# Performance work log

Hardware: AMD Instinct MI355X
Metric: run time of the kernel (lower is better)

## Reference

```python
import jax, jax.numpy as jnp
import numpy as np

EPS = 1e-5
NEG_SLOPE = 0.2  # DGL GATConv default leaky_relu slope


def conv1d_same(x, w, b):
    # x: [N, Cin, T], w: [Cout, Cin, K]
    y = jax.lax.conv_general_dilated(x, w, (1,), 'SAME',
                                     dimension_numbers=('NCW', 'OIW', 'NCW'))
    return y + b[None, :, None]


def gated_conv(x, w1, b1, w2, b2, w3, b3):
    # Temporal_Gated_Conv: relu(conv1(x)*sigmoid(conv2(x)) + conv3(x))
    return jax.nn.relu(conv1d_same(x, w1, b1) * jax.nn.sigmoid(conv1d_same(x, w2, b2))
                       + conv1d_same(x, w3, b3))


def bn3(x, g, b):
    # BatchNorm1d on [N, C, T]: stats over (N, T), training mode (batch stats)
    m = jnp.mean(x, (0, 2), keepdims=True)
    v = jnp.var(x, (0, 2), keepdims=True)
    return (x - m) * jax.lax.rsqrt(v + EPS) * g[None, :, None] + b[None, :, None]


def bn2(x, g, b):
    # BatchNorm1d on [N, F]: stats over N
    m = jnp.mean(x, 0, keepdims=True)
    v = jnp.var(x, 0, keepdims=True)
    return (x - m) * jax.lax.rsqrt(v + EPS) * g[None, :] + b[None, :]


def setup_inputs() -> dict:
    key = jax.random.key(0)
    ks = jax.random.split(key, 24)
    N, C, T, H, DEG = 20000, 32, 8, 4, 16
    F = C * T          # GAT in/out feats per head = 256
    E = N * DEG
    s = 0.05
    inp = {
        'X': jax.random.normal(ks[0], (N, C, T), jnp.float32),
        'src': jax.random.randint(ks[1], (E,), 0, N, jnp.int32),
        'dst': jax.random.randint(ks[2], (E,), 0, N, jnp.int32),
        # residual_proj: Conv1d(C->C, k=1)
        'rp_w': jax.random.normal(ks[3], (C, C, 1), jnp.float32) * s,
        'rp_b': jnp.zeros((C,), jnp.float32),
        # gated_conv1: three Conv1d(C->C, k=3)
        'g1_w1': jax.random.normal(ks[4], (C, C, 3), jnp.float32) * s,
        'g1_b1': jnp.zeros((C,), jnp.float32),
        'g1_w2': jax.random.normal(ks[5], (C, C, 3), jnp.float32) * s,
        'g1_b2': jnp.zeros((C,), jnp.float32),
        'g1_w3': jax.random.normal(ks[6], (C, C, 3), jnp.float32) * s,
        'g1_b3': jnp.zeros((C,), jnp.float32),
        'bn0_g': jnp.ones((C,), jnp.float32),
        'bn0_b': jnp.zeros((C,), jnp.float32),
        # GATConv: fc [H*F, F], attn_l/attn_r [H, F], bias [H*F]
        'gat_w': jax.random.normal(ks[7], (H * F, F), jnp.float32) * s,
        'attn_l': jax.random.normal(ks[8], (H, F), jnp.float32) * s,
        'attn_r': jax.random.normal(ks[9], (H, F), jnp.float32) * s,
        'gat_bias': jnp.zeros((H * F,), jnp.float32),
        'bn1_g': jnp.ones((H * F,), jnp.float32),
        'bn1_b': jnp.zeros((H * F,), jnp.float32),
        # gated_conv2: three Conv1d(C*H -> C, k=3)
        'g2_w1': jax.random.normal(ks[10], (C, C * H, 3), jnp.float32) * s,
        'g2_b1': jnp.zeros((C,), jnp.float32),
        'g2_w2': jax.random.normal(ks[11], (C, C * H, 3), jnp.float32) * s,
        'g2_b2': jnp.zeros((C,), jnp.float32),
        'g2_w3': jax.random.normal(ks[12], (C, C * H, 3), jnp.float32) * s,
        'g2_b3': jnp.zeros((C,), jnp.float32),
        'bn2_g': jnp.ones((C,), jnp.float32),
        'bn2_b': jnp.zeros((C,), jnp.float32),
    }
    return inp


def reference(X, src, dst, rp_w, rp_b, g1_w1, g1_b1, g1_w2, g1_b2, g1_w3, g1_b3,
              bn0_g, bn0_b, gat_w, attn_l, attn_r, gat_bias, bn1_g, bn1_b,
              g2_w1, g2_b1, g2_w2, g2_b2, g2_w3, g2_b3, bn2_g, bn2_b):
    N, C, T = X.shape
    H, F = attn_l.shape

    residual = conv1d_same(X, rp_w, rp_b)                      # [N, C, T]
    x = gated_conv(X, g1_w1, g1_b1, g1_w2, g1_b2, g1_w3, g1_b3)
    x = bn3(x, bn0_g, bn0_b)
    x = x.reshape(N, C * T)                                    # row-major flatten == torch .view

    # --- DGL GATConv (feat_drop=attn_drop=0, concat heads, ReLU activation) ---
    h = (x @ gat_w.T).reshape(N, H, F)                         # fc projection
    el = jnp.sum(h * attn_l, -1)                               # [N, H]
    er = jnp.sum(h * attn_r, -1)                               # [N, H]
    e = jax.nn.leaky_relu(el[src] + er[dst], NEG_SLOPE)        # [E, H]
    # segment softmax over incoming edges of each dst node
    m = jax.ops.segment_max(e, dst, num_segments=N)            # [N, H]
    ee = jnp.exp(e - m[dst])
    den = jax.ops.segment_sum(ee, dst, num_segments=N)         # [N, H]
    alpha = ee / den[dst]                                      # [E, H]
    rst = jax.ops.segment_sum(alpha[:, :, None] * h[src], dst, num_segments=N)  # [N, H, F]
    rst = jax.nn.relu(rst + gat_bias.reshape(H, F))

    x = rst.reshape(N, H * F)                                  # concat heads
    x = bn2(x, bn1_g, bn1_b)
    x = x.reshape(N, (H * F) // T, T)                          # [N, C*H, T]
    x = gated_conv(x, g2_w1, g2_b1, g2_w2, g2_b2, g2_w3, g2_b3)
    x = bn3(x, bn2_g, bn2_b)
    x = jax.nn.relu(x + residual)                              # self.last=True, dropout=0
    return x
```

## Files before the change

### kernel.cpp

```cpp
#include <hip/hip_runtime.h>
#include <stdint.h>

#define NN 20000
#define NE 320000

typedef unsigned short us16;
typedef __attribute__((ext_vector_type(8))) short short8;
typedef __attribute__((ext_vector_type(4))) float f32x4;

union U4 { uint4 v; us16 s[8]; unsigned u[4]; };
union U2 { uint2 v; us16 s[4]; };

__device__ __forceinline__ float b2f(us16 u){ return __uint_as_float(((unsigned)u)<<16); }
__device__ __forceinline__ us16 f2b(float f){
  unsigned u = __float_as_uint(f);
  u += 0x7fffu + ((u>>16)&1u);
  return (us16)(u>>16);
}

__global__ __launch_bounds__(256) void k_misc(
    const float* __restrict__ gatw, us16* __restrict__ Wb,
    const float* __restrict__ w1, const float* __restrict__ w2, const float* __restrict__ w3,
    us16* __restrict__ Wt,
    const float* __restrict__ c1w1, const float* __restrict__ c1w2, const float* __restrict__ c1w3,
    const float* __restrict__ rp_w, us16* __restrict__ Wt1,
    const float* __restrict__ attnl, const float* __restrict__ attnr,
    float* __restrict__ wl, float* __restrict__ wr,
    const int* __restrict__ dst, int* __restrict__ counts)
{
  const int b = blockIdx.x, tid = threadIdx.x;
  if(b < 256){
    int i = b*256 + tid;
    float4 v = *(const float4*)(gatw + (size_t)i*4);
    U2 o;
    o.s[0]=f2b(v.x); o.s[1]=f2b(v.y); o.s[2]=f2b(v.z); o.s[3]=f2b(v.w);
    *(uint2*)(Wb + (size_t)i*4) = o.v;
  } else if(b < 400){
    int i = (b-256)*256 + tid;
    int s = i/12288, rem = i%12288;
    int co3 = rem>>7, ci = rem&127;
    const float* w = (co3<32) ? w1 : (co3<64) ? w2 : w3;
    Wt[i] = f2b(w[(co3&31)*384 + ci*3 + s]);
  } else if(b < 448){
    int i = (b-400)*256 + tid;
    int s = i>>12, rem = i&4095;
    int co3 = rem>>5, ci = rem&31;
    float v;
    if(co3 < 96){
      const float* w = (co3<32) ? c1w1 : (co3<64) ? c1w2 : c1w3;
      v = w[(co3&31)*96 + ci*3 + s];
    } else {
      v = (s==1) ? rp_w[(co3-96)*32 + ci] : 0.f;
    }
    Wt1[i] = f2b(v);
  } else if(b < 456){
    int bb = b-448;
    int sel = bb>>2, hd = bb&3, k = tid;
    const float* attn = sel ? attnr : attnl;
    float s = 0.f;
    for(int f=0; f<256; f++)
      s = fmaf(attn[hd*256+f], gatw[(size_t)(hd*256+f)*256 + k], s);
    (sel ? wr : wl)[hd*256+k] = s;
  } else {
    int e = (b-456)*256 + tid;
    if(e < NE) atomicAdd(&counts[dst[e]], 1);
  }
}

__global__ __launch_bounds__(256) void k_gemm1(
    const float* __restrict__ X, const us16* __restrict__ Wt1,
    const float* __restrict__ b1, const float* __restrict__ b2, const float* __restrict__ b3,
    const float* __restrict__ rp_b,
    us16* __restrict__ gc1, us16* __restrict__ resid,
    float* __restrict__ bn0_sum, float* __restrict__ bn0_sq)
{
  __shared__ float smemF[16896];
  us16* As = (us16*)smemF;
  us16* Bs = As + 6400;
  float* Cs = smemF;
  __shared__ float redS[32], redQ[32];
  const int tid = threadIdx.x;
  if(tid<32){ redS[tid]=0.f; redQ[tid]=0.f; }
  const int node0 = blockIdx.x*16;
  const int lane = tid&63, wv = tid>>6;
  const int wm = wv&1, wn = wv>>1;
  const int mrow = lane&15, kg = (lane>>4)*8;
  for(int idx=tid; idx<1024; idx+=256){
    int n = idx>>6, rem = idx&63, slot = (rem>>5)*9, ci = rem&31;
    As[n*400 + slot*40 + ci] = 0;
  }
  #pragma unroll
  for(int i=0;i<4;i++){
    int idx = i*256 + tid;
    int n = idx>>6, rem = idx&63, ci = rem>>1, tq = rem&1;
    float4 xv = *(const float4*)(X + (size_t)(node0+n)*256 + ci*8 + tq*4);
    us16* p = &As[n*400 + (tq*4+1)*40 + ci];
    p[0]   = f2b(xv.x);
    p[40]  = f2b(xv.y);
    p[80]  = f2b(xv.z);
    p[120] = f2b(xv.w);
  }
  #pragma unroll
  for(int i=0;i<6;i++){
    int c = i*256 + tid;
    int s = c>>9, rem = c&511, co = rem>>2, cq = rem&3;
    *(uint4*)&Bs[s*5120 + co*40 + cq*8] = *(const uint4*)(Wt1 + s*4096 + co*32 + cq*8);
  }
  __syncthreads();
  f32x4 acc[4][4] = {};
  #pragma unroll
  for(int s=0; s<3; s++){
    short8 af[4], bfr[4];
    #pragma unroll
    for(int i=0;i<4;i++){
      int r = wm*64 + i*16 + mrow;
      af[i] = *(const short8*)&As[(r>>3)*400 + ((r&7)+s)*40 + kg];
    }
    #pragma unroll
    for(int j=0;j<4;j++)
      bfr[j] = *(const short8*)&Bs[s*5120 + (wn*64 + j*16 + mrow)*40 + kg];
    #pragma unroll
    for(int i=0;i<4;i++){
      #pragma unroll
      for(int j=0;j<4;j++)
        acc[i][j] = __builtin_amdgcn_mfma_f32_16x16x32_bf16(af[i], bfr[j], acc[i][j], 0, 0, 0);
    }
  }
  __syncthreads();
  #pragma unroll
  for(int i=0;i<4;i++){
    #pragma unroll
    for(int j=0;j<4;j++){
      #pragma unroll
      for(int r=0;r<4;r++)
        Cs[(wm*64 + i*16 + (lane>>4)*4 + r)*132 + wn*64 + j*16 + (lane&15)] = acc[i][j][r];
    }
  }
  __syncthreads();
  const int co = tid&31, rg = tid>>5;
  const float bb1=b1[co], bb2=b2[co], bb3=b3[co], bbr=rp_b[co];
  float s=0.f, q=0.f;
  #pragma unroll
  for(int half=0; half<2; half++){
    U4 ov, rv;
    #pragma unroll
    for(int t=0;t<8;t++){
      int r = rg*16 + half*8 + t;
      float c1 = Cs[r*132 + co]      + bb1;
      float c2 = Cs[r*132 + co + 32] + bb2;
      float c3 = Cs[r*132 + co + 64] + bb3;
      float rr = Cs[r*132 + co + 96] + bbr;
      float sg = 1.f/(1.f+__expf(-c2));
      float v = fmaf(c1, sg, c3);
      v = v>0.f ? v : 0.f;
      s += v; q += v*v;
      ov.s[t] = f2b(v);
      rv.s[t] = f2b(rr);
    }
    int node = node0 + rg*2 + half;
    *(uint4*)(gc1   + (size_t)node*256 + co*8) = ov.v;
    *(uint4*)(resid + (size_t)node*256 + co*8) = rv.v;
  }
  atomicAdd(&redS[co], s); atomicAdd(&redQ[co], q);
  __syncthreads();
  if(tid<32)      atomicAdd(&bn0_sum[tid], redS[tid]);
  else if(tid<64) atomicAdd(&bn0_sq[tid-32], redQ[tid-32]);
}

__global__ __launch_bounds__(256) void k_eler2(const us16* __restrict__ gc1,
    const float* __restrict__ bn0_sum, const float* __restrict__ bn0_sq,
    const float* __restrict__ bn0g, const float* __restrict__ bn0b,
    const float* __restrict__ wl, const float* __restrict__ wr,
    float* __restrict__ el, float* __restrict__ er)
{
  __shared__ float sa[32], sb[32];
  const int tid = threadIdx.x;
  if(tid<32){
    float m = bn0_sum[tid]*(1.f/160000.f);
    float v = bn0_sq[tid]*(1.f/160000.f) - m*m;
    float a = bn0g[tid]*rsqrtf(v + 1e-5f);
    sa[tid] = a; sb[tid] = bn0b[tid] - m*a;
  }
  __syncthreads();
  const int wv = tid>>6, lane = tid&63;
  const int node = blockIdx.x*4 + wv;
  U2 g; g.v = *(const uint2*)(gc1 + (size_t)node*256 + lane*4);
  const float a = sa[lane>>1], b = sb[lane>>1];
  float xv[4];
  #pragma unroll
  for(int j=0;j<4;j++) xv[j] = fmaf(a, b2f(g.s[j]), b);
  float res[8];
  #pragma unroll
  for(int hd=0; hd<4; hd++){
    float4 lv = *(const float4*)(wl + hd*256 + lane*4);
    float4 rv = *(const float4*)(wr + hd*256 + lane*4);
    res[hd]   = xv[0]*lv.x + xv[1]*lv.y + xv[2]*lv.z + xv[3]*lv.w;
    res[4+hd] = xv[0]*rv.x + xv[1]*rv.y + xv[2]*rv.z + xv[3]*rv.w;
  }
  #pragma unroll
  for(int o=32;o;o>>=1){
    #pragma unroll
    for(int k=0;k<8;k++) res[k] += __shfl_xor(res[k], o, 64);
  }
  if(lane==0){
    #pragma unroll
    for(int hd=0;hd<4;hd++){ el[node*4+hd]=res[hd]; er[node*4+hd]=res[4+hd]; }
  }
}

__global__ __launch_bounds__(1024) void k_scan(const int* __restrict__ counts,
                                               int* __restrict__ offsets, int* __restrict__ cursor)
{
  __shared__ int buf[1024];
  const int tid = threadIdx.x;
  const int base = tid*20;
  int loc[20];
  int s = 0;
  #pragma unroll
  for(int j=0;j<20;j++){
    int idx = base+j;
    int v = (idx<NN) ? counts[idx] : 0;
    loc[j] = s; s += v;
  }
  buf[tid] = s;
  __syncthreads();
  for(int off=1; off<1024; off<<=1){
    int t = (tid>=off) ? buf[tid-off] : 0;
    __syncthreads();
    buf[tid] += t;
    __syncthreads();
  }
  int excl = buf[tid] - s;
  #pragma unroll
  for(int j=0;j<20;j++){
    int idx = base+j;
    if(idx<NN){ offsets[idx]=excl+loc[j]; cursor[idx]=excl+loc[j]; }
  }
  if(tid==1023) offsets[NN] = excl + s;
}

__global__ __launch_bounds__(256) void k_scatter(const int* __restrict__ src, const int* __restrict__ dst,
    int* __restrict__ cursor, int* __restrict__ esrc,
    const float* __restrict__ el, const float* __restrict__ er,
    float* __restrict__ ew)
{
  int e = blockIdx.x*256 + threadIdx.x;
  if(e < NE){
    int s = src[e], d = dst[e];
    int pos = atomicAdd(&cursor[d], 1);
    esrc[pos] = s;
    float4 lv = *(const float4*)(el + s*4);
    float4 rv = *(const float4*)(er + d*4);
    float4 sc;
    sc.x = lv.x+rv.x; sc.x = sc.x>0.f ? sc.x : 0.2f*sc.x;
    sc.y = lv.y+rv.y; sc.y = sc.y>0.f ? sc.y : 0.2f*sc.y;
    sc.z = lv.z+rv.z; sc.z = sc.z>0.f ? sc.z : 0.2f*sc.z;
    sc.w = lv.w+rv.w; sc.w = sc.w>0.f ? sc.w : 0.2f*sc.w;
    *(float4*)(ew + (size_t)pos*4) = sc;
  }
}

__global__ __launch_bounds__(256) void k_agg2(
    const int* __restrict__ offsets, const int* __restrict__ esrc,
    const float* __restrict__ ew, const us16* __restrict__ gc1,
    const float* __restrict__ bn0_sum, const float* __restrict__ bn0_sq,
    const float* __restrict__ bn0g, const float* __restrict__ bn0b,
    us16* __restrict__ Axg)
{
  const int tid = threadIdx.x;
  const int wv = tid>>6, lane = tid&63;
  const int node = blockIdx.x*4 + wv;
  const int ch = lane>>1;
  float mmn = bn0_sum[ch]*(1.f/160000.f);
  float vvn = bn0_sq[ch]*(1.f/160000.f) - mmn*mmn;
  float sa = bn0g[ch]*rsqrtf(vvn + 1e-5f);
  float sb = bn0b[ch] - mmn*sa;
  const int beg = offsets[node];
  const int deg = offsets[node+1] - beg;
  const int h = lane>>4, i0 = lane&15;
  float m = -3.0e38f;
  for(int i=i0; i<deg; i+=16) m = fmaxf(m, ew[(size_t)(beg+i)*4 + h]);
  m = fmaxf(m, __shfl_xor(m,1,64)); m = fmaxf(m, __shfl_xor(m,2,64));
  m = fmaxf(m, __shfl_xor(m,4,64)); m = fmaxf(m, __shfl_xor(m,8,64));
  float den = 0.f;
  for(int i=i0; i<deg; i+=16) den += __expf(ew[(size_t)(beg+i)*4 + h] - m);
  den += __shfl_xor(den,1,64); den += __shfl_xor(den,2,64);
  den += __shfl_xor(den,4,64); den += __shfl_xor(den,8,64);
  const float m0=__shfl(m,0,64),   m1=__shfl(m,16,64),  m2=__shfl(m,32,64),  m3=__shfl(m,48,64);
  const float d0=__shfl(den,0,64), d1=__shfl(den,16,64),d2=__shfl(den,32,64),d3=__shfl(den,48,64);
  const float v0=d0>0.f?1.f/d0:0.f, v1=d1>0.f?1.f/d1:0.f,
              v2=d2>0.f?1.f/d2:0.f, v3=d3>0.f?1.f/d3:0.f;
  float a0c[4]={},a1c[4]={},a2c[4]={},a3c[4]={};
  #pragma unroll 4
  for(int j=0; j<deg; j++){
    int pos = beg+j;
    float4 w4 = *(const float4*)(ew + (size_t)pos*4);
    int sN = esrc[pos];
    U2 hv; hv.v = *(const uint2*)(gc1 + (size_t)sN*256 + lane*4);
    float e0 = __expf(w4.x-m0)*v0;
    float e1 = __expf(w4.y-m1)*v1;
    float e2 = __expf(w4.z-m2)*v2;
    float e3 = __expf(w4.w-m3)*v3;
    #pragma unroll
    for(int kk=0;kk<4;kk++){
      float x = b2f(hv.s[kk]);
      a0c[kk] = fmaf(e0,x,a0c[kk]);
      a1c[kk] = fmaf(e1,x,a1c[kk]);
      a2c[kk] = fmaf(e2,x,a2c[kk]);
      a3c[kk] = fmaf(e3,x,a3c[kk]);
    }
  }
  const float sbi = sb * ((deg>0)?1.f:0.f);
  U2 o0,o1,o2,o3;
  #pragma unroll
  for(int kk=0;kk<4;kk++){
    o0.s[kk]=f2b(fmaf(sa,a0c[kk],sbi));
    o1.s[kk]=f2b(fmaf(sa,a1c[kk],sbi));
    o2.s[kk]=f2b(fmaf(sa,a2c[kk],sbi));
    o3.s[kk]=f2b(fmaf(sa,a3c[kk],sbi));
  }
  *(uint2*)(Axg + ((size_t)node)*256            + lane*4) = o0.v;
  *(uint2*)(Axg + ((size_t)NN + node)*256       + lane*4) = o1.v;
  *(uint2*)(Axg + ((size_t)2*NN + node)*256     + lane*4) = o2.v;
  *(uint2*)(Axg + ((size_t)3*NN + node)*256     + lane*4) = o3.v;
}

__global__ __launch_bounds__(256) void k_gemm3(const us16* __restrict__ Axg, const us16* __restrict__ Wb,
    const float* __restrict__ gbias, us16* __restrict__ rst,
    float* __restrict__ bn1_sum, float* __restrict__ bn1_sq)
{
  __shared__ us16 As[128*72];
  __shared__ us16 Bs[128*72];
  const int tid = threadIdx.x;
  const int row0 = blockIdx.x*128;
  const int cb   = blockIdx.y*128;
  const int hd   = blockIdx.z;
  const us16* A = Axg + (size_t)hd*NN*256;
  const us16* B = Wb  + (size_t)(hd*256 + cb)*256;
  const int lane = tid&63, wv = tid>>6;
  const int wm = wv&1, wn = wv>>1;
  const int mrow = lane&15, kg = (lane>>4)*8;
  f32x4 acc[4][4] = {};
  for(int k0=0; k0<256; k0+=64){
    #pragma unroll
    for(int i=0;i<4;i++){
      int chunk = i*256 + tid;
      int row = chunk>>3, cc = chunk&7;
      int g = row0 + row;
      uint4 av; av.x=0;av.y=0;av.z=0;av.w=0;
      if(g < NN) av = *(const uint4*)(A + (size_t)g*256 + k0 + cc*8);
      *(uint4*)&As[row*72 + cc*8] = av;
      *(uint4*)&Bs[row*72 + cc*8] = *(const uint4*)(B + (size_t)row*256 + k0 + cc*8);
    }
    __syncthreads();
    #pragma unroll
    for(int kk=0; kk<64; kk+=32){
      short8 af[4], bfr[4];
      #pragma unroll
      for(int i=0;i<4;i++) af[i]  = *(const short8*)&As[(wm*64 + i*16 + mrow)*72 + kk + kg];
      #pragma unroll
      for(int j=0;j<4;j++) bfr[j] = *(const short8*)&Bs[(wn*64 + j*16 + mrow)*72 + kk + kg];
      #pragma unroll
      for(int i=0;i<4;i++){
        #pragma unroll
        for(int j=0;j<4;j++)
          acc[i][j] = __builtin_amdgcn_mfma_f32_16x16x32_bf16(af[i], bfr[j], acc[i][j], 0, 0, 0);
      }
    }
    __syncthreads();
  }
  float gb[4];
  #pragma unroll
  for(int j=0;j<4;j++)
    gb[j] = gbias[hd*256 + cb + wn*64 + j*16 + (lane&15)];
  float cs[4]={}, cq[4]={};
  #pragma unroll
  for(int i=0;i<4;i++){
    #pragma unroll
    for(int j=0;j<4;j++){
      #pragma unroll
      for(int r=0;r<4;r++){
        int g = row0 + wm*64 + i*16 + (lane>>4)*4 + r;
        if(g < NN){
          float v = acc[i][j][r] + gb[j];
          v = v>0.f ? v : 0.f;
          rst[(size_t)g*1024 + hd*256 + cb + wn*64 + j*16 + (lane&15)] = f2b(v);
          cs[j] += v; cq[j] += v*v;
        }
      }
    }
  }
  #pragma unroll
  for(int j=0;j<4;j++){
    cs[j] += __shfl_xor(cs[j],16,64); cs[j] += __shfl_xor(cs[j],32,64);
    cq[j] += __shfl_xor(cq[j],16,64); cq[j] += __shfl_xor(cq[j],32,64);
  }
  if(lane < 16){
    #pragma unroll
    for(int j=0;j<4;j++){
      int col = hd*256 + cb + wn*64 + j*16 + lane;
      atomicAdd(&bn1_sum[col], cs[j]);
      atomicAdd(&bn1_sq[col],  cq[j]);
    }
  }
}

__global__ __launch_bounds__(256) void k_gemm2(
    const us16* __restrict__ rst, const us16* __restrict__ Wt,
    const float* __restrict__ bn1_sum, const float* __restrict__ bn1_sq,
    const float* __restrict__ bn1g, const float* __restrict__ bn1b,
    const float* __restrict__ b1, const float* __restrict__ b2, const float* __restrict__ b3,
    us16* __restrict__ y2, float* __restrict__ bn2_sum, float* __restrict__ bn2_sq)
{
  __shared__ float smemF[16384];
  float* s1a = smemF;
  float* s1b = smemF + 1024;
  us16* As = (us16*)(smemF + 2048);
  us16* Bs = As + 21760;
  float* Cs = (float*)(smemF + 2048);
  __shared__ float redS[32], redQ[32];
  const int tid = threadIdx.x;
  if(tid<32){ redS[tid]=0.f; redQ[tid]=0.f; }
  const int node0 = blockIdx.x*16;
  const int lane = tid&63, wv = tid>>6;
  const int wm = wv&1, wn = wv>>1;
  const int mrow = lane&15, kg = (lane>>4)*8;
  for(int f=tid; f<1024; f+=256){
    float m = bn1_sum[f]*(1.f/20000.f);
    float v = bn1_sq[f]*(1.f/20000.f) - m*m;
    float a = bn1g[f]*rsqrtf(v + 1e-5f);
    int l = (f&7)*128 + (f>>3);
    s1a[l] = a; s1b[l] = bn1b[f] - m*a;
  }
  for(int idx=tid; idx<4096; idx+=256){
    int n = idx>>8, rem = idx&255, slot = (rem>>7)*9, ci = rem&127;
    As[n*1360 + slot*136 + ci] = 0;
  }
  __syncthreads();
  #pragma unroll
  for(int i=0;i<8;i++){
    int idx = i*256 + tid;
    int n = idx>>7, ci = idx&127;
    U4 in; in.v = *(const uint4*)(rst + (size_t)(node0+n)*1024 + ci*8);
    us16* p = &As[n*1360 + 136 + ci];
    #pragma unroll
    for(int t=0;t<8;t++){
      float a = s1a[t*128+ci], b = s1b[t*128+ci];
      p[t*136] = f2b(fmaf(a, b2f(in.s[t]), b));
    }
  }
  f32x4 acc[4][3] = {};
  for(int rd=0; rd<6; rd++){
    const int s = rd>>1, kc = rd&1;
    __syncthreads();
    #pragma unroll
    for(int i=0;i<3;i++){
      int chunk = i*256 + tid;
      int brow = chunk>>3, cc = chunk&7;
      *(uint4*)&Bs[brow*72 + cc*8] =
        *(const uint4*)(Wt + s*12288 + brow*128 + kc*64 + cc*8);
    }
    __syncthreads();
    #pragma unroll
    for(int kk=0; kk<64; kk+=32){
      short8 af[4], bfr[3];
      #pragma unroll
      for(int i=0;i<4;i++){
        int r = wm*64 + i*16 + mrow;
        af[i] = *(const short8*)&As[(r>>3)*1360 + ((r&7)+s)*136 + kc*64 + kk + kg];
      }
      #pragma unroll
      for(int j=0;j<3;j++)
        bfr[j] = *(const short8*)&Bs[(wn*48 + j*16 + mrow)*72 + kk + kg];
      #pragma unroll
      for(int i=0;i<4;i++){
        #pragma unroll
        for(int j=0;j<3;j++)
          acc[i][j] = __builtin_amdgcn_mfma_f32_16x16x32_bf16(af[i], bfr[j], acc[i][j], 0, 0, 0);
      }
    }
  }
  __syncthreads();
  #pragma unroll
  for(int i=0;i<4;i++){
    #pragma unroll
    for(int j=0;j<3;j++){
      #pragma unroll
      for(int r=0;r<4;r++)
        Cs[(wm*64 + i*16 + (lane>>4)*4 + r)*100 + wn*48 + j*16 + (lane&15)] = acc[i][j][r];
    }
  }
  __syncthreads();
  const int co = tid&31, rg = tid>>5;
  const float bb1=b1[co], bb2=b2[co], bb3=b3[co];
  float s=0.f, q=0.f;
  #pragma unroll
  for(int half=0; half<2; half++){
    U4 ov;
    #pragma unroll
    for(int t=0;t<8;t++){
      int r = rg*16 + half*8 + t;
      float c1 = Cs[r*100 + co]      + bb1;
      float c2 = Cs[r*100 + co + 32] + bb2;
      float c3 = Cs[r*100 + co + 64] + bb3;
      float sg = 1.f/(1.f+__expf(-c2));
      float v = fmaf(c1, sg, c3);
      v = v>0.f ? v : 0.f;
      s += v; q += v*v;
      ov.s[t] = f2b(v);
    }
    int node = node0 + rg*2 + half;
    *(uint4*)(y2 + (size_t)node*256 + co*8) = ov.v;
  }
  atomicAdd(&redS[co], s); atomicAdd(&redQ[co], q);
  __syncthreads();
  if(tid<32)      atomicAdd(&bn2_sum[tid], redS[tid]);
  else if(tid<64) atomicAdd(&bn2_sq[tid-32], redQ[tid-32]);
}

__global__ __launch_bounds__(256) void k_final(const us16* __restrict__ y2,
    const float* __restrict__ bn2_sum, const float* __restrict__ bn2_sq,
    const float* __restrict__ bn2g, const float* __restrict__ bn2b,
    const us16* __restrict__ resid, float* __restrict__ out)
{
  __shared__ float fa[32], fb[32];
  const int tid = threadIdx.x;
  if(tid<32){
    float m = bn2_sum[tid]*(1.f/160000.f);
    float v = bn2_sq[tid]*(1.f/160000.f) - m*m;
    float a = bn2g[tid]*rsqrtf(v + 1e-5f);
    fa[tid] = a; fb[tid] = bn2b[tid] - m*a;
  }
  __syncthreads();
  size_t base = ((size_t)blockIdx.x*256 + tid)*8;
  int ch = (int)((base>>3)&31);
  float a = fa[ch], b = fb[ch];
  U4 yv, rv;
  yv.v = *(const uint4*)(y2+base);
  rv.v = *(const uint4*)(resid+base);
  float4 o0, o1;
  float vv[8];
  #pragma unroll
  for(int j=0;j<8;j++){
    float v = fmaf(a, b2f(yv.s[j]), b) + b2f(rv.s[j]);
    vv[j] = v>0.f ? v : 0.f;
  }
  o0.x=vv[0]; o0.y=vv[1]; o0.z=vv[2]; o0.w=vv[3];
  o1.x=vv[4]; o1.y=vv[5]; o1.z=vv[6]; o1.w=vv[7];
  *(float4*)(out+base)   = o0;
  *(float4*)(out+base+4) = o1;
}

extern "C" void kernel_launch(void* const* d_in, const int* in_sizes, int n_in,
                              void* d_out, int out_size, void* d_ws, size_t ws_size,
                              hipStream_t stream)
{
  const float* X    = (const float*)d_in[0];
  const int*  src   = (const int*)d_in[1];
  const int*  dst   = (const int*)d_in[2];
  const float* rp_w = (const float*)d_in[3];
  const float* rp_b = (const float*)d_in[4];
  const float* g1w1 = (const float*)d_in[5];
  const float* g1b1 = (const float*)d_in[6];
  const float* g1w2 = (const float*)d_in[7];
  const float* g1b2 = (const float*)d_in[8];
  const float* g1w3 = (const float*)d_in[9];
  const float* g1b3 = (const float*)d_in[10];
  const float* bn0g = (const float*)d_in[11];
  const float* bn0b = (const float*)d_in[12];
  const float* gatw = (const float*)d_in[13];
  const float* attnl= (const float*)d_in[14];
  const float* attnr= (const float*)d_in[15];
  const float* gbias= (const float*)d_in[16];
  const float* bn1g = (const float*)d_in[17];
  const float* bn1b = (const float*)d_in[18];
  const float* g2w1 = (const float*)d_in[19];
  const float* g2b1 = (const float*)d_in[20];
  const float* g2w2 = (const float*)d_in[21];
  const float* g2b2 = (const float*)d_in[22];
  const float* g2w3 = (const float*)d_in[23];
  const float* g2b3 = (const float*)d_in[24];
  const float* bn2g = (const float*)d_in[25];
  const float* bn2b = (const float*)d_in[26];
  float* out = (float*)d_out;
  (void)in_sizes; (void)n_in; (void)out_size; (void)ws_size;

  char* w = (char*)d_ws;
  float* bn0_sum = (float*)w;
  float* bn0_sq  = bn0_sum + 32;
  float* bn1_sum = bn0_sum + 64;
  float* bn1_sq  = bn1_sum + 1024;
  float* bn2_sum = bn1_sq  + 1024;
  float* bn2_sq  = bn2_sum + 32;
  int*   counts  = (int*)(bn2_sq + 32);
  size_t zeroBytes = (size_t)((char*)(counts + NN) - w);
  int*   offsets = counts + NN;
  int*   cursor  = offsets + 20004;
  int*   esrc    = cursor + NN;
  float* el      = (float*)(esrc + NE);
  float* er      = el + NN*4;
  float* ew      = er + NN*4;
  float* wl      = ew + (size_t)NE*4;
  float* wr      = wl + 1024;
  us16*  wb      = (us16*)(wr + 1024);
  us16*  resid   = wb + 262144;
  us16*  gc1     = resid + 5120000;
  us16*  Axg     = gc1   + 5120000;
  us16*  rst     = Axg   + 20480000;
  us16*  Wt      = rst   + 20480000;
  us16*  Wt1     = Wt    + 36864;
  us16*  y2      = gc1;

  hipMemsetAsync(d_ws, 0, zeroBytes, stream);
  k_misc<<<1706, 256, 0, stream>>>(gatw, wb, g2w1, g2w2, g2w3, Wt,
                                   g1w1, g1w2, g1w3, rp_w, Wt1,
                                   attnl, attnr, wl, wr, dst, counts);
  k_gemm1<<<1250, 256, 0, stream>>>(X, Wt1, g1b1, g1b2, g1b3, rp_b,
                                    gc1, resid, bn0_sum, bn0_sq);
  k_eler2<<<5000, 256, 0, stream>>>(gc1, bn0_sum, bn0_sq, bn0g, bn0b, wl, wr, el, er);
  k_scan<<<1, 1024, 0, stream>>>(counts, offsets, cursor);
  k_scatter<<<1250, 256, 0, stream>>>(src, dst, cursor, esrc, el, er, ew);
  k_agg2<<<5000, 256, 0, stream>>>(offsets, esrc, ew, gc1, bn0_sum, bn0_sq, bn0g, bn0b, Axg);
  k_gemm3<<<dim3(157, 2, 4), 256, 0, stream>>>(Axg, wb, gbias, rst, bn1_sum, bn1_sq);
  k_gemm2<<<1250, 256, 0, stream>>>(rst, Wt, bn1_sum, bn1_sq, bn1g, bn1b,
                                    g2b1, g2b2, g2b3, y2, bn2_sum, bn2_sq);
  k_final<<<2500, 256, 0, stream>>>(y2, bn2_sum, bn2_sq, bn2g, bn2b, resid, out);
}
```

Baseline: 393.0 us.

## Fuse scan into el/er kernel, widen GAT GEMM tile to full head

The single-block prefix scan now runs as an extra block appended to the el/er kernel, which removes one launch and its serialization. The scan uses 256 threads with 79 nodes each. The GAT projection GEMM now computes a 128x256 tile per block, covering all 256 columns of a head, so each A tile is loaded once instead of twice. This doubles the accumulator registers and the B shared-memory footprint, which may reduce occupancy. An unroll pragma is also added to the attention-weight precompute loop.

```diff
diff --git a/kernel.cpp b/kernel.cpp
--- a/kernel.cpp
+++ b/kernel.cpp
@@ -58,6 +58,7 @@
     int sel = bb>>2, hd = bb&3, k = tid;
     const float* attn = sel ? attnr : attnl;
     float s = 0.f;
+    #pragma unroll 8
     for(int f=0; f<256; f++)
       s = fmaf(attn[hd*256+f], gatw[(size_t)(hd*256+f)*256 + k], s);
     (sel ? wr : wl)[hd*256+k] = s;
@@ -171,72 +172,69 @@
     const float* __restrict__ bn0_sum, const float* __restrict__ bn0_sq,
     const float* __restrict__ bn0g, const float* __restrict__ bn0b,
     const float* __restrict__ wl, const float* __restrict__ wr,
-    float* __restrict__ el, float* __restrict__ er)
-{
-  __shared__ float sa[32], sb[32];
+    float* __restrict__ el, float* __restrict__ er,
+    const int* __restrict__ counts, int* __restrict__ offsets, int* __restrict__ cursor)
+{
   const int tid = threadIdx.x;
-  if(tid<32){
-    float m = bn0_sum[tid]*(1.f/160000.f);
-    float v = bn0_sq[tid]*(1.f/160000.f) - m*m;
-    float a = bn0g[tid]*rsqrtf(v + 1e-5f);
-    sa[tid] = a; sb[tid] = bn0b[tid] - m*a;
-  }
-  __syncthreads();
-  const int wv = tid>>6, lane = tid&63;
-  const int node = blockIdx.x*4 + wv;
-  U2 g; g.v = *(const uint2*)(gc1 + (size_t)node*256 + lane*4);
-  const float a = sa[lane>>1], b = sb[lane>>1];
-  float xv[4];
-  #pragma unroll
-  for(int j=0;j<4;j++) xv[j] = fmaf(a, b2f(g.s[j]), b);
-  float res[8];
-  #pragma unroll
-  for(int hd=0; hd<4; hd++){
-    float4 lv = *(const float4*)(wl + hd*256 + lane*4);
-    float4 rv = *(const float4*)(wr + hd*256 + lane*4);
-    res[hd]   = xv[0]*lv.x + xv[1]*lv.y + xv[2]*lv.z + xv[3]*lv.w;
-    res[4+hd] = xv[0]*rv.x + xv[1]*rv.y + xv[2]*rv.z + xv[3]*rv.w;
-  }
-  #pragma unroll
-  for(int o=32;o;o>>=1){
-    #pragma unroll
-    for(int k=0;k<8;k++) res[k] += __shfl_xor(res[k], o, 64);
-  }
-  if(lane==0){
-    #pragma unroll
-    for(int hd=0;hd<4;hd++){ el[node*4+hd]=res[hd]; er[node*4+hd]=res[4+hd]; }
-  }
-}
-
-__global__ __launch_bounds__(1024) void k_scan(const int* __restrict__ counts,
-                                               int* __restrict__ offsets, int* __restrict__ cursor)
-{
-  __shared__ int buf[1024];
-  const int tid = threadIdx.x;
-  const int base = tid*20;
-  int loc[20];
-  int s = 0;
-  #pragma unroll
-  for(int j=0;j<20;j++){
-    int idx = base+j;
-    int v = (idx<NN) ? counts[idx] : 0;
-    loc[j] = s; s += v;
-  }
-  buf[tid] = s;
-  __syncthreads();
-  for(int off=1; off<1024; off<<=1){
-    int t = (tid>=off) ? buf[tid-off] : 0;
+  if(blockIdx.x < 5000){
+    __shared__ float sa[32], sb[32];
+    if(tid<32){
+      float m = bn0_sum[tid]*(1.f/160000.f);
+      float v = bn0_sq[tid]*(1.f/160000.f) - m*m;
+      float a = bn0g[tid]*rsqrtf(v + 1e-5f);
+      sa[tid] = a; sb[tid] = bn0b[tid] - m*a;
+    }
     __syncthreads();
-    buf[tid] += t;
+    const int wv = tid>>6, lane = tid&63;
+    const int node = blockIdx.x*4 + wv;
+    U2 g; g.v = *(const uint2*)(gc1 + (size_t)node*256 + lane*4);
+    const float a = sa[lane>>1], b = sb[lane>>1];
+    float xv[4];
+    #pragma unroll
+    for(int j=0;j<4;j++) xv[j] = fmaf(a, b2f(g.s[j]), b);
+    float res[8];
+    #pragma unroll
+    for(int hd=0; hd<4; hd++){
+      float4 lv = *(const float4*)(wl + hd*256 + lane*4);
+      float4 rv = *(const float4*)(wr + hd*256 + lane*4);
+      res[hd]   = xv[0]*lv.x + xv[1]*lv.y + xv[2]*lv.z + xv[3]*lv.w;
+      res[4+hd] = xv[0]*rv.x + xv[1]*rv.y + xv[2]*rv.z + xv[3]*rv.w;
+    }
+    #pragma unroll
+    for(int o=32;o;o>>=1){
+      #pragma unroll
+      for(int k=0;k<8;k++) res[k] += __shfl_xor(res[k], o, 64);
+    }
+    if(lane==0){
+      #pragma unroll
+      for(int hd=0;hd<4;hd++){ el[node*4+hd]=res[hd]; er[node*4+hd]=res[4+hd]; }
+    }
+  } else {
+    __shared__ int buf[256];
+    const int base = tid*79;
+    int s = 0;
+    for(int j=0;j<79;j++){
+      int idx = base+j;
+      if(idx<NN) s += counts[idx];
+    }
+    buf[tid] = s;
     __syncthreads();
-  }
-  int excl = buf[tid] - s;
-  #pragma unroll
-  for(int j=0;j<20;j++){
-    int idx = base+j;
-    if(idx<NN){ offsets[idx]=excl+loc[j]; cursor[idx]=excl+loc[j]; }
-  }
-  if(tid==1023) offsets[NN] = excl + s;
+    for(int off=1; off<256; off<<=1){
+      int t = (tid>=off) ? buf[tid-off] : 0;
+      __syncthreads();
+      buf[tid] += t;
+      __syncthreads();
+    }
+    int excl = buf[tid] - s;
+    for(int j=0;j<79;j++){
+      int idx = base+j;
+      if(idx<NN){
+        offsets[idx]=excl; cursor[idx]=excl;
+        excl += counts[idx];
+      }
+    }
+    if(tid==255) offsets[NN] = buf[255];
+  }
 }
 
 __global__ __launch_bounds__(256) void k_scatter(const int* __restrict__ src, const int* __restrict__ dst,
@@ -330,17 +328,16 @@
     float* __restrict__ bn1_sum, float* __restrict__ bn1_sq)
 {
   __shared__ us16 As[128*72];
-  __shared__ us16 Bs[128*72];
+  __shared__ us16 Bs[256*72];
   const int tid = threadIdx.x;
   const int row0 = blockIdx.x*128;
-  const int cb   = blockIdx.y*128;
-  const int hd   = blockIdx.z;
+  const int hd   = blockIdx.y;
   const us16* A = Axg + (size_t)hd*NN*256;
-  const us16* B = Wb  + (size_t)(hd*256 + cb)*256;
+  const us16* B = Wb  + (size_t)hd*256*256;
   const int lane = tid&63, wv = tid>>6;
   const int wm = wv&1, wn = wv>>1;
   const int mrow = lane&15, kg = (lane>>4)*8;
-  f32x4 acc[4][4] = {};
+  f32x4 acc[4][8] = {};
   for(int k0=0; k0<256; k0+=64){
     #pragma unroll
     for(int i=0;i<4;i++){
@@ -350,55 +347,60 @@
       uint4 av; av.x=0;av.y=0;av.z=0;av.w=0;
       if(g < NN) av = *(const uint4*)(A + (size_t)g*256 + k0 + cc*8);
       *(uint4*)&As[row*72 + cc*8] = av;
+    }
+    #pragma unroll
+    for(int i=0;i<8;i++){
+      int chunk = i*256 + tid;
+      int row = chunk>>3, cc = chunk&7;
       *(uint4*)&Bs[row*72 + cc*8] = *(const uint4*)(B + (size_t)row*256 + k0 + cc*8);
     }
     __syncthreads();
     #pragma unroll
     for(int kk=0; kk<64; kk+=32){
-      short8 af[4], bfr[4];
+      short8 af[4], bfr[8];
       #pragma unroll
       for(int i=0;i<4;i++) af[i]  = *(const short8*)&As[(wm*64 + i*16 + mrow)*72 + kk + kg];
       #pragma unroll
-      for(int j=0;j<4;j++) bfr[j] = *(const short8*)&Bs[(wn*64 + j*16 + mrow)*72 + kk + kg];
+      for(int j=0;j<8;j++) bfr[j] = *(const short8*)&Bs[(wn*128 + j*16 + mrow)*72 + kk + kg];
       #pragma unroll
       for(int i=0;i<4;i++){
         #pragma unroll
-        for(int j=0;j<4;j++)
+        for(int j=0;j<8;j++)
           acc[i][j] = __builtin_amdgcn_mfma_f32_16x16x32_bf16(af[i], bfr[j], acc[i][j], 0, 0, 0);
       }
     }
     __syncthreads();
   }
-  float gb[4];
-  #pragma unroll
-  for(int j=0;j<4;j++)
-    gb[j] = gbias[hd*256 + cb + wn*64 + j*16 + (lane&15)];
-  float cs[4]={}, cq[4]={};
+  float gb[8];
+  #pragma unroll
+  for(int j=0;j<8;j++)
+    gb[j] = gbias[hd*256 + wn*128 + j*16 + (lane&15)];
+  float cs[8]={}, cq[8]={};
   #pragma unroll
   for(int i=0;i<4;i++){
     #pragma unroll
-    for(int j=0;j<4;j++){
+    for(int j=0;j<8;j++){
       #pragma unroll
       for(int r=0;r<4;r++){
         int g = row0 + wm*64 + i*16 + (lane>>4)*4 + r;
         if(g < NN){
           float v = acc[i][j][r] + gb[j];
           v = v>0.f ? v : 0.f;
-          rst[(size_t)g*1024 + hd*256 + cb + wn*64 + j*16 + (lane&15)] = f2b(v);
+          rst[(size_t)g*1024 + hd*256 + wn*128 + j*16 + (lane&15)] = f2b(v);
           cs[j] += v; cq[j] += v*v;
         }
       }
     }
   }
   #pragma unroll
-  for(int j=0;j<4;j++){
+  for(int j=0;j<8;j++){
     cs[j] += __shfl_xor(cs[j],16,64); cs[j] += __shfl_xor(cs[j],32,64);
     cq[j] += __shfl_xor(cq[j],16,64); cq[j] += __shfl_xor(cq[j],32,64);
   }
   if(lane < 16){
     #pragma unroll
-    for(int j=0;j<4;j++){
-      int col = hd*256 + cb + wn*64 + j*16 + lane;
+    for(int j=0;j<8;j++){
+      int col = hd*256 + wn*128 + j*16 + lane;
       atomicAdd(&bn1_sum[col], cs[j]);
       atomicAdd(&bn1_sq[col],  cq[j]);
     }
@@ -617,11 +619,11 @@
                                    attnl, attnr, wl, wr, dst, counts);
   k_gemm1<<<1250, 256, 0, stream>>>(X, Wt1, g1b1, g1b2, g1b3, rp_b,
                                     gc1, resid, bn0_sum, bn0_sq);
-  k_eler2<<<5000, 256, 0, stream>>>(gc1, bn0_sum, bn0_sq, bn0g, bn0b, wl, wr, el, er);
-  k_scan<<<1, 1024, 0, stream>>>(counts, offsets, cursor);
+  k_eler2<<<5001, 256, 0, stream>>>(gc1, bn0_sum, bn0_sq, bn0g, bn0b, wl, wr, el, er,
+                                    counts, offsets, cursor);
   k_scatter<<<1250, 256, 0, stream>>>(src, dst, cursor, esrc, el, er, ew);
   k_agg2<<<5000, 256, 0, stream>>>(offsets, esrc, ew, gc1, bn0_sum, bn0_sq, bn0g, bn0b, Axg);
-  k_gemm3<<<dim3(157, 2, 4), 256, 0, stream>>>(Axg, wb, gbias, rst, bn1_sum, bn1_sq);
+  k_gemm3<<<dim3(157, 4), 256, 0, stream>>>(Axg, wb, gbias, rst, bn1_sum, bn1_sq);
   k_gemm2<<<1250, 256, 0, stream>>>(rst, Wt, bn1_sum, bn1_sq, bn1g, bn1b,
                                     g2b1, g2b2, g2b3, y2, bn2_sum, bn2_sq);
   k_final<<<2500, 256, 0, stream>>>(y2, bn2_sum, bn2_sq, bn2g, bn2b, resid, out);
```

Measured after the change: 445.3 us. 1.13x slower.

## Fuse scan into eler kernel, split attn-weight reduction, shrink gemm3 K tile

Applied to the files above, without the earlier changes.

The single-block scan is folded into the el/er kernel as an extra block, which removes one kernel launch. It now uses 256 threads instead of 1024 and does a serial 79-element pass that rereads counts. The attention-weight folding in k_misc is split four ways over f, with atomicAdd into wl/wr, which are moved into the zeroed workspace region. gemm3 now uses a 32-wide K tile with smaller shared-memory buffers, which may raise occupancy but doubles the number of barriers.

```diff
diff --git a/kernel.cpp b/kernel.cpp
--- a/kernel.cpp
+++ b/kernel.cpp
@@ -53,16 +53,19 @@
       v = (s==1) ? rp_w[(co3-96)*32 + ci] : 0.f;
     }
     Wt1[i] = f2b(v);
-  } else if(b < 456){
+  } else if(b < 480){
     int bb = b-448;
-    int sel = bb>>2, hd = bb&3, k = tid;
+    int sel = bb>>4, hd = (bb>>2)&3, fq = bb&3;
     const float* attn = sel ? attnr : attnl;
+    int k = tid;
     float s = 0.f;
-    for(int f=0; f<256; f++)
+    int f0 = fq*64;
+    #pragma unroll 8
+    for(int f=f0; f<f0+64; f++)
       s = fmaf(attn[hd*256+f], gatw[(size_t)(hd*256+f)*256 + k], s);
-    (sel ? wr : wl)[hd*256+k] = s;
+    atomicAdd(&((sel ? wr : wl)[hd*256+k]), s);
   } else {
-    int e = (b-456)*256 + tid;
+    int e = (b-480)*256 + tid;
     if(e < NE) atomicAdd(&counts[dst[e]], 1);
   }
 }
@@ -171,72 +174,69 @@
     const float* __restrict__ bn0_sum, const float* __restrict__ bn0_sq,
     const float* __restrict__ bn0g, const float* __restrict__ bn0b,
     const float* __restrict__ wl, const float* __restrict__ wr,
-    float* __restrict__ el, float* __restrict__ er)
-{
-  __shared__ float sa[32], sb[32];
+    float* __restrict__ el, float* __restrict__ er,
+    const int* __restrict__ counts, int* __restrict__ offsets, int* __restrict__ cursor)
+{
   const int tid = threadIdx.x;
-  if(tid<32){
-    float m = bn0_sum[tid]*(1.f/160000.f);
-    float v = bn0_sq[tid]*(1.f/160000.f) - m*m;
-    float a = bn0g[tid]*rsqrtf(v + 1e-5f);
-    sa[tid] = a; sb[tid] = bn0b[tid] - m*a;
-  }
-  __syncthreads();
-  const int wv = tid>>6, lane = tid&63;
-  const int node = blockIdx.x*4 + wv;
-  U2 g; g.v = *(const uint2*)(gc1 + (size_t)node*256 + lane*4);
-  const float a = sa[lane>>1], b = sb[lane>>1];
-  float xv[4];
-  #pragma unroll
-  for(int j=0;j<4;j++) xv[j] = fmaf(a, b2f(g.s[j]), b);
-  float res[8];
-  #pragma unroll
-  for(int hd=0; hd<4; hd++){
-    float4 lv = *(const float4*)(wl + hd*256 + lane*4);
-    float4 rv = *(const float4*)(wr + hd*256 + lane*4);
-    res[hd]   = xv[0]*lv.x + xv[1]*lv.y + xv[2]*lv.z + xv[3]*lv.w;
-    res[4+hd] = xv[0]*rv.x + xv[1]*rv.y + xv[2]*rv.z + xv[3]*rv.w;
-  }
-  #pragma unroll
-  for(int o=32;o;o>>=1){
-    #pragma unroll
-    for(int k=0;k<8;k++) res[k] += __shfl_xor(res[k], o, 64);
-  }
-  if(lane==0){
-    #pragma unroll
-    for(int hd=0;hd<4;hd++){ el[node*4+hd]=res[hd]; er[node*4+hd]=res[4+hd]; }
-  }
-}
-
-__global__ __launch_bounds__(1024) void k_scan(const int* __restrict__ counts,
-                                               int* __restrict__ offsets, int* __restrict__ cursor)
-{
-  __shared__ int buf[1024];
-  const int tid = threadIdx.x;
-  const int base = tid*20;
-  int loc[20];
-  int s = 0;
-  #pragma unroll
-  for(int j=0;j<20;j++){
-    int idx = base+j;
-    int v = (idx<NN) ? counts[idx] : 0;
-    loc[j] = s; s += v;
-  }
-  buf[tid] = s;
-  __syncthreads();
-  for(int off=1; off<1024; off<<=1){
-    int t = (tid>=off) ? buf[tid-off] : 0;
+  if(blockIdx.x < 5000){
+    __shared__ float sa[32], sb[32];
+    if(tid<32){
+      float m = bn0_sum[tid]*(1.f/160000.f);
+      float v = bn0_sq[tid]*(1.f/160000.f) - m*m;
+      float a = bn0g[tid]*rsqrtf(v + 1e-5f);
+      sa[tid] = a; sb[tid] = bn0b[tid] - m*a;
+    }
     __syncthreads();
-    buf[tid] += t;
+    const int wv = tid>>6, lane = tid&63;
+    const int node = blockIdx.x*4 + wv;
+    U2 g; g.v = *(const uint2*)(gc1 + (size_t)node*256 + lane*4);
+    const float a = sa[lane>>1], b = sb[lane>>1];
+    float xv[4];
+    #pragma unroll
+    for(int j=0;j<4;j++) xv[j] = fmaf(a, b2f(g.s[j]), b);
+    float res[8];
+    #pragma unroll
+    for(int hd=0; hd<4; hd++){
+      float4 lv = *(const float4*)(wl + hd*256 + lane*4);
+      float4 rv = *(const float4*)(wr + hd*256 + lane*4);
+      res[hd]   = xv[0]*lv.x + xv[1]*lv.y + xv[2]*lv.z + xv[3]*lv.w;
+      res[4+hd] = xv[0]*rv.x + xv[1]*rv.y + xv[2]*rv.z + xv[3]*rv.w;
+    }
+    #pragma unroll
+    for(int o=32;o;o>>=1){
+      #pragma unroll
+      for(int k=0;k<8;k++) res[k] += __shfl_xor(res[k], o, 64);
+    }
+    if(lane==0){
+      #pragma unroll
+      for(int hd=0;hd<4;hd++){ el[node*4+hd]=res[hd]; er[node*4+hd]=res[4+hd]; }
+    }
+  } else {
+    __shared__ int buf[256];
+    const int base = tid*79;
+    int s = 0;
+    for(int j=0;j<79;j++){
+      int idx = base+j;
+      if(idx<NN) s += counts[idx];
+    }
+    buf[tid] = s;
     __syncthreads();
-  }
-  int excl = buf[tid] - s;
-  #pragma unroll
-  for(int j=0;j<20;j++){
-    int idx = base+j;
-    if(idx<NN){ offsets[idx]=excl+loc[j]; cursor[idx]=excl+loc[j]; }
-  }
-  if(tid==1023) offsets[NN] = excl + s;
+    for(int off=1; off<256; off<<=1){
+      int t = (tid>=off) ? buf[tid-off] : 0;
+      __syncthreads();
+      buf[tid] += t;
+      __syncthreads();
+    }
+    int excl = buf[tid] - s;
+    for(int j=0;j<79;j++){
+      int idx = base+j;
+      if(idx<NN){
+        offsets[idx]=excl; cursor[idx]=excl;
+        excl += counts[idx];
+      }
+    }
+    if(tid==255) offsets[NN] = buf[255];
+  }
 }
 
 __global__ __launch_bounds__(256) void k_scatter(const int* __restrict__ src, const int* __restrict__ dst,
@@ -329,8 +329,8 @@
     const float* __restrict__ gbias, us16* __restrict__ rst,
     float* __restrict__ bn1_sum, float* __restrict__ bn1_sq)
 {
-  __shared__ us16 As[128*72];
-  __shared__ us16 Bs[128*72];
+  __shared__ us16 As[128*40];
+  __shared__ us16 Bs[128*40];
   const int tid = threadIdx.x;
   const int row0 = blockIdx.x*128;
   const int cb   = blockIdx.y*128;
@@ -341,31 +341,28 @@
   const int wm = wv&1, wn = wv>>1;
   const int mrow = lane&15, kg = (lane>>4)*8;
   f32x4 acc[4][4] = {};
-  for(int k0=0; k0<256; k0+=64){
-    #pragma unroll
-    for(int i=0;i<4;i++){
+  for(int k0=0; k0<256; k0+=32){
+    #pragma unroll
+    for(int i=0;i<2;i++){
       int chunk = i*256 + tid;
-      int row = chunk>>3, cc = chunk&7;
+      int row = chunk>>2, cc = chunk&3;
       int g = row0 + row;
       uint4 av; av.x=0;av.y=0;av.z=0;av.w=0;
       if(g < NN) av = *(const uint4*)(A + (size_t)g*256 + k0 + cc*8);
-      *(uint4*)&As[row*72 + cc*8] = av;
-      *(uint4*)&Bs[row*72 + cc*8] = *(const uint4*)(B + (size_t)row*256 + k0 + cc*8);
+      *(uint4*)&As[row*40 + cc*8] = av;
+      *(uint4*)&Bs[row*40 + cc*8] = *(const uint4*)(B + (size_t)row*256 + k0 + cc*8);
     }
     __syncthreads();
-    #pragma unroll
-    for(int kk=0; kk<64; kk+=32){
-      short8 af[4], bfr[4];
-      #pragma unroll
-      for(int i=0;i<4;i++) af[i]  = *(const short8*)&As[(wm*64 + i*16 + mrow)*72 + kk + kg];
-      #pragma unroll
-      for(int j=0;j<4;j++) bfr[j] = *(const short8*)&Bs[(wn*64 + j*16 + mrow)*72 + kk + kg];
-      #pragma unroll
-      for(int i=0;i<4;i++){
-        #pragma unroll
-        for(int j=0;j<4;j++)
-          acc[i][j] = __builtin_amdgcn_mfma_f32_16x16x32_bf16(af[i], bfr[j], acc[i][j], 0, 0, 0);
-      }
+    short8 af[4], bfr[4];
+    #pragma unroll
+    for(int i=0;i<4;i++) af[i]  = *(const short8*)&As[(wm*64 + i*16 + mrow)*40 + kg];
+    #pragma unroll
+    for(int j=0;j<4;j++) bfr[j] = *(const short8*)&Bs[(wn*64 + j*16 + mrow)*40 + kg];
+    #pragma unroll
+    for(int i=0;i<4;i++){
+      #pragma unroll
+      for(int j=0;j<4;j++)
+        acc[i][j] = __builtin_amdgcn_mfma_f32_16x16x32_bf16(af[i], bfr[j], acc[i][j], 0, 0, 0);
     }
     __syncthreads();
   }
@@ -592,7 +589,9 @@
   float* bn1_sq  = bn1_sum + 1024;
   float* bn2_sum = bn1_sq  + 1024;
   float* bn2_sq  = bn2_sum + 32;
-  int*   counts  = (int*)(bn2_sq + 32);
+  float* wl      = bn2_sq + 32;
+  float* wr      = wl + 1024;
+  int*   counts  = (int*)(wr + 1024);
   size_t zeroBytes = (size_t)((char*)(counts + NN) - w);
   int*   offsets = counts + NN;
   int*   cursor  = offsets + 20004;
@@ -600,9 +599,7 @@
   float* el      = (float*)(esrc + NE);
   float* er      = el + NN*4;
   float* ew      = er + NN*4;
-  float* wl      = ew + (size_t)NE*4;
-  float* wr      = wl + 1024;
-  us16*  wb      = (us16*)(wr + 1024);
+  us16*  wb      = (us16*)(ew + (size_t)NE*4);
   us16*  resid   = wb + 262144;
   us16*  gc1     = resid + 5120000;
   us16*  Axg     = gc1   + 5120000;
@@ -612,13 +609,13 @@
   us16*  y2      = gc1;
 
   hipMemsetAsync(d_ws, 0, zeroBytes, stream);
-  k_misc<<<1706, 256, 0, stream>>>(gatw, wb, g2w1, g2w2, g2w3, Wt,
+  k_misc<<<1730, 256, 0, stream>>>(gatw, wb, g2w1, g2w2, g2w3, Wt,
                                    g1w1, g1w2, g1w3, rp_w, Wt1,
                                    attnl, attnr, wl, wr, dst, counts);
   k_gemm1<<<1250, 256, 0, stream>>>(X, Wt1, g1b1, g1b2, g1b3, rp_b,
                                     gc1, resid, bn0_sum, bn0_sq);
-  k_eler2<<<5000, 256, 0, stream>>>(gc1, bn0_sum, bn0_sq, bn0g, bn0b, wl, wr, el, er);
-  k_scan<<<1, 1024, 0, stream>>>(counts, offsets, cursor);
+  k_eler2<<<5001, 256, 0, stream>>>(gc1, bn0_sum, bn0_sq, bn0g, bn0b, wl, wr, el, er,
+                                    counts, offsets, cursor);
   k_scatter<<<1250, 256, 0, stream>>>(src, dst, cursor, esrc, el, er, ew);
   k_agg2<<<5000, 256, 0, stream>>>(offsets, esrc, ew, gc1, bn0_sum, bn0_sq, bn0g, bn0b, Axg);
   k_gemm3<<<dim3(157, 2, 4), 256, 0, stream>>>(Axg, wb, gbias, rst, bn1_sum, bn1_sq);
```

Measured after the change: 401.9 us. +2.3%, slower.
